# Optimization experiments

Measured on AMD Instinct MI355X. Metric: run time of the kernel, lower is better.

The kernel has to match this reference:

```python
import jax, jax.numpy as jnp
import numpy as np
import math

HIDDEN = 1024
NUM_LAYERS = 24
INIT_RANGE = 0.02


def setup_inputs() -> dict:
    key = jax.random.key(0)
    k1, k2 = jax.random.split(key)
    B, S, H = 4, 4096, HIDDEN
    hidden_states = jax.random.normal(k1, (B, S, H), dtype=jnp.float32)
    std = INIT_RANGE / math.sqrt(2.0 * NUM_LAYERS * H)
    # queries weight: [H, H], applied as F.linear => x @ W^T
    W_q = jax.random.normal(k2, (H, H), dtype=jnp.float32) * std
    return {"hidden_states": hidden_states, "W_q": W_q}


def reference(hidden_states, W_q):
    # queries = F.linear(x, W) = x @ W^T          [B, S, H]
    q = jnp.einsum('bsh,oh->bso', hidden_states, W_q)
    # pre_attn = Q @ K^T where K = x             [B, S, S]
    pre_attn = jnp.einsum('bso,bto->bst', q, hidden_states)
    # attention = pre_attn @ V where V = x       [B, S, H]
    attention = jnp.einsum('bst,bth->bsh', pre_attn, hidden_states)
    return attention
```

## Files before the change

kernel.cpp:

```cpp
#include <hip/hip_runtime.h>
#include <hip/hip_bf16.h>
#include <stdint.h>

#define H_DIM 1024
#define S_DIM 4096
#define B_DIM 4

typedef __bf16 bf16x8 __attribute__((ext_vector_type(8)));
typedef float f32x4 __attribute__((ext_vector_type(4)));
typedef unsigned short u16x4 __attribute__((ext_vector_type(4)));
typedef unsigned short u16x8 __attribute__((ext_vector_type(8)));

__device__ __forceinline__ unsigned short f2bf(float f) {
    union { float f; uint32_t u; } v; v.f = f;
    uint32_t u = v.u;
    uint32_t r = (u + 0x7FFFu + ((u >> 16) & 1u)) >> 16;
    return (unsigned short)r;
}
__device__ __forceinline__ float bf2f(unsigned short u) {
    union { uint32_t u; float f; } v; v.u = (uint32_t)u << 16; return v.f;
}

__device__ __forceinline__ void wg_barrier() {
    asm volatile("s_barrier" ::: "memory");
}

template <int IMM>
__device__ __forceinline__ bf16x8 ds_read_b128_imm(unsigned addr) {
    bf16x8 r;
    asm volatile("ds_read_b128 %0, %1 offset:%2"
                 : "=v"(r) : "v"(addr), "i"(IMM));
    return r;
}

__global__ __launch_bounds__(256)
void cast_x_kernel(const float* __restrict__ X,
                   unsigned short* __restrict__ Xb,
                   unsigned short* __restrict__ XT) {
    __shared__ float tile[64][65];
    const int b  = blockIdx.z;
    const int h0 = blockIdx.x * 64;
    const int s0 = blockIdx.y * 64;
    const int tx = threadIdx.x;
    const int ty = threadIdx.y;
#pragma unroll
    for (int j = 0; j < 4; ++j) {
        int s = ty + 16 * j;
        f32x4 v = *(const f32x4*)&X[((size_t)b * S_DIM + s0 + s) * H_DIM + h0 + tx * 4];
        u16x4 o;
#pragma unroll
        for (int k = 0; k < 4; ++k) {
            tile[s][tx * 4 + k] = v[k];
            o[k] = f2bf(v[k]);
        }
        *(u16x4*)&Xb[((size_t)b * S_DIM + s0 + s) * H_DIM + h0 + tx * 4] = o;
    }
    __syncthreads();
#pragma unroll
    for (int j = 0; j < 4; ++j) {
        int hh = ty + 16 * j;
        u16x4 o;
#pragma unroll
        for (int k = 0; k < 4; ++k)
            o[k] = f2bf(tile[tx * 4 + k][hh]);
        *(u16x4*)&XT[((size_t)b * H_DIM + h0 + hh) * S_DIM + s0 + tx * 4] = o;
    }
}

__global__ void cast_w_kernel(const float* __restrict__ W,
                              unsigned short* __restrict__ WT) {
    __shared__ float tile[32][33];
    const int b0 = blockIdx.x * 32;
    const int o0 = blockIdx.y * 32;
    const int tx = threadIdx.x;
    const int ty = threadIdx.y;
#pragma unroll
    for (int i = 0; i < 4; ++i) {
        int o = ty + 8 * i;
        tile[o][tx] = W[(size_t)(o0 + o) * H_DIM + b0 + tx];
    }
    __syncthreads();
#pragma unroll
    for (int i = 0; i < 4; ++i) {
        int bb = ty + 8 * i;
        WT[(size_t)(b0 + bb) * H_DIM + o0 + tx] = f2bf(tile[tx][bb]);
    }
}

template <int NSPLIT>
__global__ void reduce_cast_u16_kernel(const unsigned short* __restrict__ P,
                                       unsigned short* __restrict__ Out,
                                       size_t sSplit) {
    size_t i = ((size_t)blockIdx.x * blockDim.x + threadIdx.x) * 8;
    float s[8] = {0.f, 0.f, 0.f, 0.f, 0.f, 0.f, 0.f, 0.f};
#pragma unroll
    for (int sp = 0; sp < NSPLIT; ++sp) {
        u16x8 u = *(const u16x8*)&P[(size_t)sp * sSplit + i];
#pragma unroll
        for (int k = 0; k < 8; ++k) s[k] += bf2f(u[k]);
    }
    u16x8 o;
#pragma unroll
    for (int k = 0; k < 8; ++k) o[k] = f2bf(s[k]);
    *(u16x8*)&Out[i] = o;
}

template <typename OutT, int NSPLIT>
__global__ __launch_bounds__(512, 2)
void gemm_q4_kernel(const unsigned short* __restrict__ A,
                    const unsigned short* __restrict__ Bt,
                    OutT* __restrict__ C,
                    int K, int lda, int ldb, int ldc,
                    size_t sA, size_t sB, size_t sC, size_t sSplit) {
    extern __shared__ char smem_raw[];

    const int tid  = threadIdx.x;
    const int w    = tid >> 6;
    const int lane = tid & 63;
    const int wm   = w & 1;
    const int wn   = w >> 1;
    const int q    = lane >> 4;
    const int col  = lane & 15;

    const int tileM = blockIdx.x * 256;
    const int tileN = blockIdx.y * 256;
    const int bz   = blockIdx.z / NSPLIT;
    const int sp   = blockIdx.z % NSPLIT;
    const int Ksub = K / NSPLIT;
    const int T    = Ksub >> 5;

    const unsigned short* Ab = A + sA * bz + (size_t)sp * Ksub;
    const unsigned short* Bb = Bt + sB * bz + (size_t)sp * Ksub;

    auto lds3 = (__attribute__((address_space(3))) char*)&smem_raw[0];
    const unsigned ldsBase = (unsigned)(size_t)lds3;

    const unsigned aBase = ldsBase + (unsigned)(q * 4096 + wm * 2048 + col * 16);
    const unsigned bBase = ldsBase + 16384u + (unsigned)(q * 4096 + wn * 1024 + col * 16);

    const unsigned short* srcA[2];
    const unsigned short* srcB[2];
    int dstOf[2];
#pragma unroll
    for (int j = 0; j < 2; ++j) {
        int c = 2 * w + j;
        int k8l = c >> 2, r64 = c & 3;
        srcA[j] = Ab + (size_t)(tileM + r64 * 64 + lane) * lda + k8l * 8;
        srcB[j] = Bb + (size_t)(tileN + r64 * 64 + lane) * ldb + k8l * 8;
        dstOf[j] = (k8l * 256 + r64 * 64) * 16;
    }

    auto stageA = [&](int buf) {
#pragma unroll
        for (int j = 0; j < 2; ++j) {
            __builtin_amdgcn_global_load_lds(
                (const __attribute__((address_space(1))) void*)srcA[j],
                (__attribute__((address_space(3))) void*)(lds3 + buf * 32768 + dstOf[j]),
                16, 0, 0);
            srcA[j] += 32;
        }
    };
    auto stageB = [&](int buf) {
#pragma unroll
        for (int j = 0; j < 2; ++j) {
            __builtin_amdgcn_global_load_lds(
                (const __attribute__((address_space(1))) void*)srcB[j],
                (__attribute__((address_space(3))) void*)(lds3 + buf * 32768 + 16384 + dstOf[j]),
                16, 0, 0);
            srcB[j] += 32;
        }
    };

    f32x4 acc[8][4];
#pragma unroll
    for (int r = 0; r < 8; ++r)
#pragma unroll
        for (int c = 0; c < 4; ++c)
            acc[r][c] = (f32x4){0.f, 0.f, 0.f, 0.f};

    stageA(0); stageB(0);
    stageA(1); stageB(1);
    stageA(2); stageB(2);

    for (int n = 0; n < T; ++n) {
        if (n <= T - 3)      asm volatile("s_waitcnt vmcnt(8)" ::: "memory");
        else if (n == T - 2) asm volatile("s_waitcnt vmcnt(4)" ::: "memory");
        else                 asm volatile("s_waitcnt vmcnt(0)" ::: "memory");
        wg_barrier();

        if (n + 3 < T) { stageA((n + 3) & 3); stageB((n + 3) & 3); }

        const unsigned aAddr = aBase + (unsigned)((n & 3) << 15);
        const unsigned bAddr = bBase + (unsigned)((n & 3) << 15);
        bf16x8 av[8], bv[4];

        av[0] = ds_read_b128_imm<0>(aAddr);
        av[1] = ds_read_b128_imm<256>(aAddr);
        av[2] = ds_read_b128_imm<512>(aAddr);
        av[3] = ds_read_b128_imm<768>(aAddr);
        bv[0] = ds_read_b128_imm<0>(bAddr);
        bv[1] = ds_read_b128_imm<256>(bAddr);
        bv[2] = ds_read_b128_imm<512>(bAddr);
        bv[3] = ds_read_b128_imm<768>(bAddr);
        av[4] = ds_read_b128_imm<1024>(aAddr);
        av[5] = ds_read_b128_imm<1280>(aAddr);
        av[6] = ds_read_b128_imm<1536>(aAddr);
        av[7] = ds_read_b128_imm<1792>(aAddr);

        asm volatile("s_waitcnt lgkmcnt(4)" ::: "memory");
        __builtin_amdgcn_sched_barrier(0);
        __builtin_amdgcn_s_setprio(1);
#pragma unroll
        for (int mf = 0; mf < 4; ++mf)
#pragma unroll
            for (int nf = 0; nf < 4; ++nf)
                acc[mf][nf] = __builtin_amdgcn_mfma_f32_16x16x32_bf16(
                    av[mf], bv[nf], acc[mf][nf], 0, 0, 0);
        __builtin_amdgcn_s_setprio(0);

        asm volatile("s_waitcnt lgkmcnt(0)" ::: "memory");
        __builtin_amdgcn_sched_barrier(0);
        __builtin_amdgcn_s_setprio(1);
#pragma unroll
        for (int mf = 0; mf < 4; ++mf)
#pragma unroll
            for (int nf = 0; nf < 4; ++nf)
                acc[4 + mf][nf] = __builtin_amdgcn_mfma_f32_16x16x32_bf16(
                    av[4 + mf], bv[nf], acc[4 + mf][nf], 0, 0, 0);
        __builtin_amdgcn_s_setprio(0);
    }

    OutT* Cb = C + sC * bz + sSplit * sp;
    __syncthreads();
    float* lws = (float*)(smem_raw) + (size_t)w * 1088;
    const int lr = lane >> 4;
    const int lc = lane & 15;
#pragma unroll
    for (int mf = 0; mf < 8; ++mf) {
#pragma unroll
        for (int nf = 0; nf < 4; ++nf)
#pragma unroll
            for (int v = 0; v < 4; ++v)
                lws[(q * 4 + v) * 68 + nf * 16 + col] = acc[mf][nf][v];
#pragma unroll
        for (int p = 0; p < 4; ++p) {
            f32x4 t = *(const f32x4*)&lws[(p * 4 + lr) * 68 + lc * 4];
            int row  = tileM + wm * 128 + mf * 16 + p * 4 + lr;
            int colg = tileN + wn * 64 + lc * 4;
            if constexpr (sizeof(OutT) == 2) {
                u16x4 u;
                u[0] = f2bf(t[0]); u[1] = f2bf(t[1]);
                u[2] = f2bf(t[2]); u[3] = f2bf(t[3]);
                *(u16x4*)&Cb[(size_t)row * ldc + colg] = u;
            } else {
                *(f32x4*)&Cb[(size_t)row * ldc + colg] = t;
            }
        }
    }
}

extern "C" void kernel_launch(void* const* d_in, const int* in_sizes, int n_in,
                              void* d_out, int out_size, void* d_ws, size_t ws_size,
                              hipStream_t stream) {
    const float* X = (const float*)d_in[0];
    const float* W = (const float*)d_in[1];
    float* out = (float*)d_out;

    char* ws = (char*)d_ws;
    unsigned short* Xb = (unsigned short*)(ws);
    unsigned short* XT = (unsigned short*)(ws + 33554432);
    unsigned short* WT = (unsigned short*)(ws + 67108864);
    unsigned short* G  = (unsigned short*)(ws + 69206016);
    unsigned short* MT = (unsigned short*)(ws + 77594624);
    unsigned short* Gpart  = (unsigned short*)(ws + 85983232);
    unsigned short* MTpart = (unsigned short*)(ws + 85983232);

    const size_t sBH = (size_t)B_DIM * H_DIM * H_DIM;

    cast_x_kernel<<<dim3(H_DIM / 64, S_DIM / 64, B_DIM), dim3(16, 16), 0, stream>>>(X, Xb, XT);
    cast_w_kernel<<<dim3(H_DIM / 32, H_DIM / 32, 1), dim3(32, 8), 0, stream>>>(W, WT);

    gemm_q4_kernel<unsigned short, 4><<<dim3(4, 4, B_DIM * 4), 512, 131072, stream>>>(
        XT, XT, Gpart, S_DIM, S_DIM, S_DIM, H_DIM,
        (size_t)H_DIM * S_DIM, (size_t)H_DIM * S_DIM, (size_t)H_DIM * H_DIM, sBH);
    reduce_cast_u16_kernel<4><<<dim3(sBH / 8 / 256), 256, 0, stream>>>(Gpart, G, sBH);

    gemm_q4_kernel<unsigned short, 4><<<dim3(4, 4, B_DIM * 4), 512, 131072, stream>>>(
        G, WT, MTpart, H_DIM, H_DIM, H_DIM, H_DIM,
        (size_t)H_DIM * H_DIM, (size_t)0, (size_t)H_DIM * H_DIM, sBH);
    reduce_cast_u16_kernel<4><<<dim3(sBH / 8 / 256), 256, 0, stream>>>(MTpart, MT, sBH);

    gemm_q4_kernel<float, 1><<<dim3(S_DIM / 256, H_DIM / 256, B_DIM), 512, 131072, stream>>>(
        Xb, MT, out, H_DIM, H_DIM, H_DIM, H_DIM,
        (size_t)S_DIM * H_DIM, (size_t)H_DIM * H_DIM, (size_t)S_DIM * H_DIM, 0);
}
```

Measured before the change: 262.3 us.

## Switch GEMM to BK=64 double buffer with interleaved half-tile prefetch

Restructures the GEMM main loop from a 4-stage ring of K=32 tiles to two K=64 buffers, each split into two 32-wide halves. Prefetches of the next tile's halves are issued between the LDS reads and MFMA groups, with a barrier per half. This halves the outer iteration count and spreads global-to-LDS traffic across the compute phases, but the prefetch distance drops from three stages to one, so global latency may be exposed more often.

```diff
diff --git a/kernel.cpp b/kernel.cpp
--- a/kernel.cpp
+++ b/kernel.cpp
@@ -107,7 +107,7 @@
 
 template <typename OutT, int NSPLIT>
 __global__ __launch_bounds__(512, 2)
-void gemm_q4_kernel(const unsigned short* __restrict__ A,
+void gemm_p5_kernel(const unsigned short* __restrict__ A,
                     const unsigned short* __restrict__ Bt,
                     OutT* __restrict__ C,
                     int K, int lda, int ldb, int ldc,
@@ -127,7 +127,7 @@
     const int bz   = blockIdx.z / NSPLIT;
     const int sp   = blockIdx.z % NSPLIT;
     const int Ksub = K / NSPLIT;
-    const int T    = Ksub >> 5;
+    const int T    = Ksub >> 6;
 
     const unsigned short* Ab = A + sA * bz + (size_t)sp * Ksub;
     const unsigned short* Bb = Bt + sB * bz + (size_t)sp * Ksub;
@@ -135,40 +135,34 @@
     auto lds3 = (__attribute__((address_space(3))) char*)&smem_raw[0];
     const unsigned ldsBase = (unsigned)(size_t)lds3;
 
-    const unsigned aBase = ldsBase + (unsigned)(q * 4096 + wm * 2048 + col * 16);
-    const unsigned bBase = ldsBase + 16384u + (unsigned)(q * 4096 + wn * 1024 + col * 16);
-
-    const unsigned short* srcA[2];
-    const unsigned short* srcB[2];
-    int dstOf[2];
+    const unsigned aBase = ldsBase + (unsigned)(q * 4096 + (wm * 128 + col) * 16);
+    const unsigned bBase = ldsBase + 32768u + (unsigned)(q * 4096 + (wn * 64 + col) * 16);
+
+    const unsigned short* pA[2];
+    const unsigned short* pB[2];
+    unsigned dstA[2];
 #pragma unroll
     for (int j = 0; j < 2; ++j) {
-        int c = 2 * w + j;
-        int k8l = c >> 2, r64 = c & 3;
-        srcA[j] = Ab + (size_t)(tileM + r64 * 64 + lane) * lda + k8l * 8;
-        srcB[j] = Bb + (size_t)(tileN + r64 * 64 + lane) * ldb + k8l * 8;
-        dstOf[j] = (k8l * 256 + r64 * 64) * 16;
-    }
-
-    auto stageA = [&](int buf) {
-#pragma unroll
-        for (int j = 0; j < 2; ++j) {
+        int c = 2 * w + j, k8r = c >> 2, r64 = c & 3;
+        pA[j] = Ab + (size_t)(tileM + r64 * 64 + lane) * lda + k8r * 8;
+        pB[j] = Bb + (size_t)(tileN + r64 * 64 + lane) * ldb + k8r * 8;
+        dstA[j] = (unsigned)(k8r * 4096 + r64 * 1024);
+    }
+    auto stageA = [&](int tgt, int h) {
+#pragma unroll
+        for (int j = 0; j < 2; ++j)
             __builtin_amdgcn_global_load_lds(
-                (const __attribute__((address_space(1))) void*)srcA[j],
-                (__attribute__((address_space(3))) void*)(lds3 + buf * 32768 + dstOf[j]),
+                (const __attribute__((address_space(1))) void*)(pA[j] + tgt * 64 + h * 32),
+                (__attribute__((address_space(3))) void*)(lds3 + ((unsigned)(tgt & 1) * 65536u + dstA[j] + (unsigned)h * 16384u)),
                 16, 0, 0);
-            srcA[j] += 32;
-        }
     };
-    auto stageB = [&](int buf) {
-#pragma unroll
-        for (int j = 0; j < 2; ++j) {
+    auto stageB = [&](int tgt, int h) {
+#pragma unroll
+        for (int j = 0; j < 2; ++j)
             __builtin_amdgcn_global_load_lds(
-                (const __attribute__((address_space(1))) void*)srcB[j],
-                (__attribute__((address_space(3))) void*)(lds3 + buf * 32768 + 16384 + dstOf[j]),
+                (const __attribute__((address_space(1))) void*)(pB[j] + tgt * 64 + h * 32),
+                (__attribute__((address_space(3))) void*)(lds3 + ((unsigned)(tgt & 1) * 65536u + 32768u + dstA[j] + (unsigned)h * 16384u)),
                 16, 0, 0);
-            srcB[j] += 32;
-        }
     };
 
     f32x4 acc[8][4];
@@ -178,21 +172,16 @@
         for (int c = 0; c < 4; ++c)
             acc[r][c] = (f32x4){0.f, 0.f, 0.f, 0.f};
 
-    stageA(0); stageB(0);
-    stageA(1); stageB(1);
-    stageA(2); stageB(2);
+    stageA(0, 0); stageB(0, 0); stageA(0, 1); stageB(0, 1);
 
     for (int n = 0; n < T; ++n) {
-        if (n <= T - 3)      asm volatile("s_waitcnt vmcnt(8)" ::: "memory");
-        else if (n == T - 2) asm volatile("s_waitcnt vmcnt(4)" ::: "memory");
-        else                 asm volatile("s_waitcnt vmcnt(0)" ::: "memory");
+        const unsigned aAddr = aBase + (unsigned)((n & 1) << 16);
+        const unsigned bAddr = bBase + (unsigned)((n & 1) << 16);
+        const bool pf = (n + 1 < T);
+        bf16x8 av[4], bv[4];
+
+        asm volatile("s_waitcnt vmcnt(4)" ::: "memory");
         wg_barrier();
-
-        if (n + 3 < T) { stageA((n + 3) & 3); stageB((n + 3) & 3); }
-
-        const unsigned aAddr = aBase + (unsigned)((n & 3) << 15);
-        const unsigned bAddr = bBase + (unsigned)((n & 3) << 15);
-        bf16x8 av[8], bv[4];
 
         av[0] = ds_read_b128_imm<0>(aAddr);
         av[1] = ds_read_b128_imm<256>(aAddr);
@@ -202,12 +191,8 @@
         bv[1] = ds_read_b128_imm<256>(bAddr);
         bv[2] = ds_read_b128_imm<512>(bAddr);
         bv[3] = ds_read_b128_imm<768>(bAddr);
-        av[4] = ds_read_b128_imm<1024>(aAddr);
-        av[5] = ds_read_b128_imm<1280>(aAddr);
-        av[6] = ds_read_b128_imm<1536>(aAddr);
-        av[7] = ds_read_b128_imm<1792>(aAddr);
-
-        asm volatile("s_waitcnt lgkmcnt(4)" ::: "memory");
+        if (pf) stageA(n + 1, 0);
+        asm volatile("s_waitcnt lgkmcnt(0)" ::: "memory");
         __builtin_amdgcn_sched_barrier(0);
         __builtin_amdgcn_s_setprio(1);
 #pragma unroll
@@ -218,6 +203,11 @@
                     av[mf], bv[nf], acc[mf][nf], 0, 0, 0);
         __builtin_amdgcn_s_setprio(0);
 
+        av[0] = ds_read_b128_imm<1024>(aAddr);
+        av[1] = ds_read_b128_imm<1280>(aAddr);
+        av[2] = ds_read_b128_imm<1536>(aAddr);
+        av[3] = ds_read_b128_imm<1792>(aAddr);
+        if (pf) stageB(n + 1, 0);
         asm volatile("s_waitcnt lgkmcnt(0)" ::: "memory");
         __builtin_amdgcn_sched_barrier(0);
         __builtin_amdgcn_s_setprio(1);
@@ -226,7 +216,47 @@
 #pragma unroll
             for (int nf = 0; nf < 4; ++nf)
                 acc[4 + mf][nf] = __builtin_amdgcn_mfma_f32_16x16x32_bf16(
-                    av[4 + mf], bv[nf], acc[4 + mf][nf], 0, 0, 0);
+                    av[mf], bv[nf], acc[4 + mf][nf], 0, 0, 0);
+        __builtin_amdgcn_s_setprio(0);
+
+        if (pf) asm volatile("s_waitcnt vmcnt(4)" ::: "memory");
+        else    asm volatile("s_waitcnt vmcnt(0)" ::: "memory");
+        wg_barrier();
+
+        av[0] = ds_read_b128_imm<16384 + 0>(aAddr);
+        av[1] = ds_read_b128_imm<16384 + 256>(aAddr);
+        av[2] = ds_read_b128_imm<16384 + 512>(aAddr);
+        av[3] = ds_read_b128_imm<16384 + 768>(aAddr);
+        bv[0] = ds_read_b128_imm<16384 + 0>(bAddr);
+        bv[1] = ds_read_b128_imm<16384 + 256>(bAddr);
+        bv[2] = ds_read_b128_imm<16384 + 512>(bAddr);
+        bv[3] = ds_read_b128_imm<16384 + 768>(bAddr);
+        if (pf) stageA(n + 1, 1);
+        asm volatile("s_waitcnt lgkmcnt(0)" ::: "memory");
+        __builtin_amdgcn_sched_barrier(0);
+        __builtin_amdgcn_s_setprio(1);
+#pragma unroll
+        for (int mf = 0; mf < 4; ++mf)
+#pragma unroll
+            for (int nf = 0; nf < 4; ++nf)
+                acc[mf][nf] = __builtin_amdgcn_mfma_f32_16x16x32_bf16(
+                    av[mf], bv[nf], acc[mf][nf], 0, 0, 0);
+        __builtin_amdgcn_s_setprio(0);
+
+        av[0] = ds_read_b128_imm<16384 + 1024>(aAddr);
+        av[1] = ds_read_b128_imm<16384 + 1280>(aAddr);
+        av[2] = ds_read_b128_imm<16384 + 1536>(aAddr);
+        av[3] = ds_read_b128_imm<16384 + 1792>(aAddr);
+        if (pf) stageB(n + 1, 1);
+        asm volatile("s_waitcnt lgkmcnt(0)" ::: "memory");
+        __builtin_amdgcn_sched_barrier(0);
+        __builtin_amdgcn_s_setprio(1);
+#pragma unroll
+        for (int mf = 0; mf < 4; ++mf)
+#pragma unroll
+            for (int nf = 0; nf < 4; ++nf)
+                acc[4 + mf][nf] = __builtin_amdgcn_mfma_f32_16x16x32_bf16(
+                    av[mf], bv[nf], acc[4 + mf][nf], 0, 0, 0);
         __builtin_amdgcn_s_setprio(0);
     }
 
@@ -280,17 +310,17 @@
     cast_x_kernel<<<dim3(H_DIM / 64, S_DIM / 64, B_DIM), dim3(16, 16), 0, stream>>>(X, Xb, XT);
     cast_w_kernel<<<dim3(H_DIM / 32, H_DIM / 32, 1), dim3(32, 8), 0, stream>>>(W, WT);
 
-    gemm_q4_kernel<unsigned short, 4><<<dim3(4, 4, B_DIM * 4), 512, 131072, stream>>>(
+    gemm_p5_kernel<unsigned short, 4><<<dim3(4, 4, B_DIM * 4), 512, 131072, stream>>>(
         XT, XT, Gpart, S_DIM, S_DIM, S_DIM, H_DIM,
         (size_t)H_DIM * S_DIM, (size_t)H_DIM * S_DIM, (size_t)H_DIM * H_DIM, sBH);
     reduce_cast_u16_kernel<4><<<dim3(sBH / 8 / 256), 256, 0, stream>>>(Gpart, G, sBH);
 
-    gemm_q4_kernel<unsigned short, 4><<<dim3(4, 4, B_DIM * 4), 512, 131072, stream>>>(
+    gemm_p5_kernel<unsigned short, 4><<<dim3(4, 4, B_DIM * 4), 512, 131072, stream>>>(
         G, WT, MTpart, H_DIM, H_DIM, H_DIM, H_DIM,
         (size_t)H_DIM * H_DIM, (size_t)0, (size_t)H_DIM * H_DIM, sBH);
     reduce_cast_u16_kernel<4><<<dim3(sBH / 8 / 256), 256, 0, stream>>>(MTpart, MT, sBH);
 
-    gemm_q4_kernel<float, 1><<<dim3(S_DIM / 256, H_DIM / 256, B_DIM), 512, 131072, stream>>>(
+    gemm_p5_kernel<float, 1><<<dim3(S_DIM / 256, H_DIM / 256, B_DIM), 512, 131072, stream>>>(
         Xb, MT, out, H_DIM, H_DIM, H_DIM, H_DIM,
         (size_t)S_DIM * H_DIM, (size_t)H_DIM * H_DIM, (size_t)S_DIM * H_DIM, 0);
 }
```

New measurement: 258.5 us. Within noise of the previous version (-1.5%).

## Shrink GEMM tiles to 128x128 with 256 threads and 3-stage LDS pipeline

Applied to the files above, without the earlier changes.

Replaces the 256x256, 512-thread GEMM with 4-stage LDS buffering by a 128x128, 256-thread tile using a triple buffer (48KB of LDS) that targets three blocks per CU. The grids grow by four times, which raises parallelism and occupancy for the small split-K GEMMs, and a swap flag changes the block-to-tile mapping order. In exchange, each block reuses less data per staged tile, so more global and L2 traffic goes through LDS. The s_setprio hints and the split LDS-read wait are also removed.

```diff
diff --git a/kernel.cpp b/kernel.cpp
--- a/kernel.cpp
+++ b/kernel.cpp
@@ -105,9 +105,9 @@
     *(u16x8*)&Out[i] = o;
 }
 
-template <typename OutT, int NSPLIT>
-__global__ __launch_bounds__(512, 2)
-void gemm_q4_kernel(const unsigned short* __restrict__ A,
+template <typename OutT, int NSPLIT, bool SWAPXY>
+__global__ __launch_bounds__(256, 3)
+void gemm_t3_kernel(const unsigned short* __restrict__ A,
                     const unsigned short* __restrict__ Bt,
                     OutT* __restrict__ C,
                     int K, int lda, int ldb, int ldc,
@@ -122,8 +122,14 @@
     const int q    = lane >> 4;
     const int col  = lane & 15;
 
-    const int tileM = blockIdx.x * 256;
-    const int tileN = blockIdx.y * 256;
+    int tileM, tileN;
+    if constexpr (SWAPXY) {
+        tileM = blockIdx.x * 128;
+        tileN = blockIdx.y * 128;
+    } else {
+        tileN = blockIdx.x * 128;
+        tileM = blockIdx.y * 128;
+    }
     const int bz   = blockIdx.z / NSPLIT;
     const int sp   = blockIdx.z % NSPLIT;
     const int Ksub = K / NSPLIT;
@@ -135,65 +141,57 @@
     auto lds3 = (__attribute__((address_space(3))) char*)&smem_raw[0];
     const unsigned ldsBase = (unsigned)(size_t)lds3;
 
-    const unsigned aBase = ldsBase + (unsigned)(q * 4096 + wm * 2048 + col * 16);
-    const unsigned bBase = ldsBase + 16384u + (unsigned)(q * 4096 + wn * 1024 + col * 16);
-
-    const unsigned short* srcA[2];
-    const unsigned short* srcB[2];
-    int dstOf[2];
+    const unsigned aBase = ldsBase + (unsigned)(q * 2048 + (wm * 64 + col) * 16);
+    const unsigned bBase = ldsBase + 8192u + (unsigned)(q * 2048 + (wn * 64 + col) * 16);
+
+    const unsigned short* pA[2];
+    const unsigned short* pB[2];
+    unsigned dstOf[2];
 #pragma unroll
     for (int j = 0; j < 2; ++j) {
-        int c = 2 * w + j;
-        int k8l = c >> 2, r64 = c & 3;
-        srcA[j] = Ab + (size_t)(tileM + r64 * 64 + lane) * lda + k8l * 8;
-        srcB[j] = Bb + (size_t)(tileN + r64 * 64 + lane) * ldb + k8l * 8;
-        dstOf[j] = (k8l * 256 + r64 * 64) * 16;
-    }
-
-    auto stageA = [&](int buf) {
-#pragma unroll
-        for (int j = 0; j < 2; ++j) {
+        int c = 2 * w + j, k8 = c >> 1, r64 = c & 1;
+        pA[j] = Ab + (size_t)(tileM + r64 * 64 + lane) * lda + k8 * 8;
+        pB[j] = Bb + (size_t)(tileN + r64 * 64 + lane) * ldb + k8 * 8;
+        dstOf[j] = (unsigned)((k8 * 128 + r64 * 64) * 16);
+    }
+    auto stage = [&](int tgt, int buf) {
+        unsigned bo = (unsigned)buf * 16384u;
+#pragma unroll
+        for (int j = 0; j < 2; ++j)
             __builtin_amdgcn_global_load_lds(
-                (const __attribute__((address_space(1))) void*)srcA[j],
-                (__attribute__((address_space(3))) void*)(lds3 + buf * 32768 + dstOf[j]),
+                (const __attribute__((address_space(1))) void*)(pA[j] + tgt * 32),
+                (__attribute__((address_space(3))) void*)(lds3 + bo + dstOf[j]),
                 16, 0, 0);
-            srcA[j] += 32;
-        }
+#pragma unroll
+        for (int j = 0; j < 2; ++j)
+            __builtin_amdgcn_global_load_lds(
+                (const __attribute__((address_space(1))) void*)(pB[j] + tgt * 32),
+                (__attribute__((address_space(3))) void*)(lds3 + bo + 8192u + dstOf[j]),
+                16, 0, 0);
     };
-    auto stageB = [&](int buf) {
-#pragma unroll
-        for (int j = 0; j < 2; ++j) {
-            __builtin_amdgcn_global_load_lds(
-                (const __attribute__((address_space(1))) void*)srcB[j],
-                (__attribute__((address_space(3))) void*)(lds3 + buf * 32768 + 16384 + dstOf[j]),
-                16, 0, 0);
-            srcB[j] += 32;
-        }
-    };
-
-    f32x4 acc[8][4];
-#pragma unroll
-    for (int r = 0; r < 8; ++r)
+
+    f32x4 acc[4][4];
+#pragma unroll
+    for (int r = 0; r < 4; ++r)
 #pragma unroll
         for (int c = 0; c < 4; ++c)
             acc[r][c] = (f32x4){0.f, 0.f, 0.f, 0.f};
 
-    stageA(0); stageB(0);
-    stageA(1); stageB(1);
-    stageA(2); stageB(2);
-
+    stage(0, 0);
+    stage(1, 1);
+
+    int buf = 0;
+    int nbuf = 2;
     for (int n = 0; n < T; ++n) {
-        if (n <= T - 3)      asm volatile("s_waitcnt vmcnt(8)" ::: "memory");
-        else if (n == T - 2) asm volatile("s_waitcnt vmcnt(4)" ::: "memory");
-        else                 asm volatile("s_waitcnt vmcnt(0)" ::: "memory");
+        if (n + 1 < T) asm volatile("s_waitcnt vmcnt(4)" ::: "memory");
+        else           asm volatile("s_waitcnt vmcnt(0)" ::: "memory");
         wg_barrier();
 
-        if (n + 3 < T) { stageA((n + 3) & 3); stageB((n + 3) & 3); }
-
-        const unsigned aAddr = aBase + (unsigned)((n & 3) << 15);
-        const unsigned bAddr = bBase + (unsigned)((n & 3) << 15);
-        bf16x8 av[8], bv[4];
-
+        if (n + 2 < T) stage(n + 2, nbuf);
+
+        const unsigned aAddr = aBase + (unsigned)(buf * 16384);
+        const unsigned bAddr = bBase + (unsigned)(buf * 16384);
+        bf16x8 av[4], bv[4];
         av[0] = ds_read_b128_imm<0>(aAddr);
         av[1] = ds_read_b128_imm<256>(aAddr);
         av[2] = ds_read_b128_imm<512>(aAddr);
@@ -202,32 +200,17 @@
         bv[1] = ds_read_b128_imm<256>(bAddr);
         bv[2] = ds_read_b128_imm<512>(bAddr);
         bv[3] = ds_read_b128_imm<768>(bAddr);
-        av[4] = ds_read_b128_imm<1024>(aAddr);
-        av[5] = ds_read_b128_imm<1280>(aAddr);
-        av[6] = ds_read_b128_imm<1536>(aAddr);
-        av[7] = ds_read_b128_imm<1792>(aAddr);
-
-        asm volatile("s_waitcnt lgkmcnt(4)" ::: "memory");
+        asm volatile("s_waitcnt lgkmcnt(0)" ::: "memory");
         __builtin_amdgcn_sched_barrier(0);
-        __builtin_amdgcn_s_setprio(1);
 #pragma unroll
         for (int mf = 0; mf < 4; ++mf)
 #pragma unroll
             for (int nf = 0; nf < 4; ++nf)
                 acc[mf][nf] = __builtin_amdgcn_mfma_f32_16x16x32_bf16(
                     av[mf], bv[nf], acc[mf][nf], 0, 0, 0);
-        __builtin_amdgcn_s_setprio(0);
-
-        asm volatile("s_waitcnt lgkmcnt(0)" ::: "memory");
-        __builtin_amdgcn_sched_barrier(0);
-        __builtin_amdgcn_s_setprio(1);
-#pragma unroll
-        for (int mf = 0; mf < 4; ++mf)
-#pragma unroll
-            for (int nf = 0; nf < 4; ++nf)
-                acc[4 + mf][nf] = __builtin_amdgcn_mfma_f32_16x16x32_bf16(
-                    av[4 + mf], bv[nf], acc[4 + mf][nf], 0, 0, 0);
-        __builtin_amdgcn_s_setprio(0);
+
+        buf  = (buf == 2)  ? 0 : buf + 1;
+        nbuf = (nbuf == 2) ? 0 : nbuf + 1;
     }
 
     OutT* Cb = C + sC * bz + sSplit * sp;
@@ -236,7 +219,7 @@
     const int lr = lane >> 4;
     const int lc = lane & 15;
 #pragma unroll
-    for (int mf = 0; mf < 8; ++mf) {
+    for (int mf = 0; mf < 4; ++mf) {
 #pragma unroll
         for (int nf = 0; nf < 4; ++nf)
 #pragma unroll
@@ -245,7 +228,7 @@
 #pragma unroll
         for (int p = 0; p < 4; ++p) {
             f32x4 t = *(const f32x4*)&lws[(p * 4 + lr) * 68 + lc * 4];
-            int row  = tileM + wm * 128 + mf * 16 + p * 4 + lr;
+            int row  = tileM + wm * 64 + mf * 16 + p * 4 + lr;
             int colg = tileN + wn * 64 + lc * 4;
             if constexpr (sizeof(OutT) == 2) {
                 u16x4 u;
@@ -280,17 +263,17 @@
     cast_x_kernel<<<dim3(H_DIM / 64, S_DIM / 64, B_DIM), dim3(16, 16), 0, stream>>>(X, Xb, XT);
     cast_w_kernel<<<dim3(H_DIM / 32, H_DIM / 32, 1), dim3(32, 8), 0, stream>>>(W, WT);
 
-    gemm_q4_kernel<unsigned short, 4><<<dim3(4, 4, B_DIM * 4), 512, 131072, stream>>>(
+    gemm_t3_kernel<unsigned short, 4, false><<<dim3(8, 8, B_DIM * 4), 256, 49152, stream>>>(
         XT, XT, Gpart, S_DIM, S_DIM, S_DIM, H_DIM,
         (size_t)H_DIM * S_DIM, (size_t)H_DIM * S_DIM, (size_t)H_DIM * H_DIM, sBH);
     reduce_cast_u16_kernel<4><<<dim3(sBH / 8 / 256), 256, 0, stream>>>(Gpart, G, sBH);
 
-    gemm_q4_kernel<unsigned short, 4><<<dim3(4, 4, B_DIM * 4), 512, 131072, stream>>>(
+    gemm_t3_kernel<unsigned short, 4, false><<<dim3(8, 8, B_DIM * 4), 256, 49152, stream>>>(
         G, WT, MTpart, H_DIM, H_DIM, H_DIM, H_DIM,
         (size_t)H_DIM * H_DIM, (size_t)0, (size_t)H_DIM * H_DIM, sBH);
     reduce_cast_u16_kernel<4><<<dim3(sBH / 8 / 256), 256, 0, stream>>>(MTpart, MT, sBH);
 
-    gemm_q4_kernel<float, 1><<<dim3(S_DIM / 256, H_DIM / 256, B_DIM), 512, 131072, stream>>>(
+    gemm_t3_kernel<float, 1, true><<<dim3(S_DIM / 128, H_DIM / 128, B_DIM), 256, 49152, stream>>>(
         Xb, MT, out, H_DIM, H_DIM, H_DIM, H_DIM,
         (size_t)S_DIM * H_DIM, (size_t)H_DIM * H_DIM, (size_t)S_DIM * H_DIM, 0);
 }
```

After: 293.8 us. 1.12x slower.
